# Optimization experiments

Hardware: AMD Instinct MI355X
Metric: run time of the kernel (lower is better)

Reference implementation:

```python
import jax, jax.numpy as jnp
import numpy as np

BETA = 0.5      # conf.beta (undefined global in original repo)
ALPHA = 0.2     # LeakyReLU negative slope (init arg alpha)
N, E, FIN, FOUT = 50000, 1_600_000, 128, 64


def setup_inputs() -> dict:
    key = jax.random.key(0)
    k1, k2, k3, k4, k5 = jax.random.split(key, 5)
    inp = jax.random.normal(k1, (N, FIN), dtype=jnp.float32)
    edge = jax.random.randint(k2, (2, E), 0, N)                      # [2,E] (src,dst), = adj.nonzero().t()
    M_vals = jax.random.uniform(k3, (E,), dtype=jnp.float32)          # M gathered at edges
    # xavier_normal with gain 1.414, matching torch init
    W = jax.random.normal(k4, (FIN, FOUT), dtype=jnp.float32) * (1.414 * np.sqrt(2.0 / (FIN + FOUT)))
    a = jax.random.normal(k5, (2 * FOUT,), dtype=jnp.float32) * (1.414 * np.sqrt(2.0 / (1 + 2 * FOUT)))
    return {"input": inp, "M_vals": M_vals, "W": W, "a": a, "edge": edge}


def reference(input, M_vals, W, a, edge):
    n, f = input.shape[0], W.shape[1]
    src, dst = edge[0], edge[1]
    h = input @ W                                   # [N, F]
    # M = beta*M + (1-beta)*adj; at edges adj == 1
    bias = M_vals * BETA + (1.0 - BETA)             # [E]
    # a . cat(h_src, bias*h_dst) == (h@a[:F])[src] + bias * (h@a[F:])[dst]
    s1 = h @ a[:f]                                  # [N]
    s2 = h @ a[f:]                                  # [N]
    edge_e = jnp.exp(jax.nn.leaky_relu(s1[src] + bias * s2[dst], negative_slope=ALPHA))  # [E]
    # special_spmm(edge, e, [N,N], ones) -> per-row sum of edge weights
    e_rowsum = jax.ops.segment_sum(edge_e, src, num_segments=n)       # [N]
    # special_spmm(edge, e, [N,N], h) -> weighted aggregation of dst features into src rows
    h_prime = jax.ops.segment_sum(edge_e[:, None] * h[dst], src, num_segments=n)  # [N, F]
    h_prime = h_prime / e_rowsum[:, None]
    return jax.nn.elu(h_prime)                      # concat=True
```

## Files before the change

### kernel.cpp

```cpp
#include <hip/hip_runtime.h>
#include <hip/hip_bf16.h>

#define NN   50000
#define EE   1600000
#define FIN  128
#define FOUT 64
#define BETA  0.5f
#define ALPHA 0.2f
#define SBW    256
#define NB2    196
#define RCAP   9000
#define PGRID  400
#define PCHUNK 4000
#define CAP2   9008
#define XS     136

typedef __attribute__((ext_vector_type(8))) short short8;
typedef __attribute__((ext_vector_type(8))) unsigned short ushort8v;
typedef __attribute__((ext_vector_type(4))) float float4v;

__device__ __forceinline__ float load_any(const void* p, long i, int isf32) {
    if (isf32) return ((const float*)p)[i];
    unsigned int b = ((unsigned int)(((const unsigned short*)p)[i])) << 16;
    return __uint_as_float(b);
}

__device__ __forceinline__ unsigned short f32_to_bf16_rne(float f) {
    unsigned int b = __float_as_uint(f);
    return (unsigned short)((b + 0x7FFF + ((b >> 16) & 1)) >> 16);
}

__device__ __forceinline__ float bf16_to_f32(unsigned short u) {
    return __uint_as_float(((unsigned int)u) << 16);
}

__global__ __launch_bounds__(256) void detect_kernel(
    const void* inp, const void* Mv, const void* W, const void* a, int* flags)
{
    const void* ptrs[4] = { inp, Mv, W, a };
    const long  cnts[4] = { (long)NN * FIN, (long)EE, (long)FIN * FOUT, 2L * FOUT };
    const int t = blockIdx.x;
    const unsigned short* p = (const unsigned short*)ptrs[t];
    const long half = cnts[t] >> 1;
    long step = half / 256; if (step == 0) step = 1;
    const long pos = 2 * (((long)threadIdx.x * step) % half);

    const float v = bf16_to_f32(p[pos]);
    const int bad = (isnan(v) || fabsf(v) > 1e4f) ? 1 : 0;

    __shared__ int sbad[256];
    sbad[threadIdx.x] = bad;
    __syncthreads();
    for (int s = 128; s > 0; s >>= 1) {
        if (threadIdx.x < (unsigned)s) sbad[threadIdx.x] |= sbad[threadIdx.x + s];
        __syncthreads();
    }
    if (threadIdx.x == 0) flags[t] = sbad[0];
}

__global__ __launch_bounds__(256) void wt_kernel(
    const void* __restrict__ W, const int* __restrict__ flags,
    unsigned short* __restrict__ Wt, int* __restrict__ bcur)
{
    if (blockIdx.x == 0 && threadIdx.x < NB2) bcur[threadIdx.x] = 0;
    const int fW = flags[2];
    const int i = blockIdx.x * 256 + threadIdx.x;
    if (i < FIN * FOUT) {
        const int k = i >> 6, n = i & 63;
        Wt[n * FIN + k] = f32_to_bf16_rne(load_any(W, i, fW));
    }
}

__global__ __launch_bounds__(256) void mfma_gemm_kernel(
    const void* __restrict__ inp,
    const unsigned short* __restrict__ Wt,
    const void* __restrict__ a,
    const int* __restrict__ flags,
    unsigned short* __restrict__ h,
    float* __restrict__ s1,
    float* __restrict__ s2)
{
    __shared__ unsigned short Xs[16 * XS];
    __shared__ float part1[4][16];
    __shared__ float part2[4][16];

    const int tid  = threadIdx.x;
    const int wave = tid >> 6;
    const int lane = tid & 63;
    const int quad = lane >> 4;
    const int col  = lane & 15;
    const int rb   = blockIdx.x * 16;

    const int fI = flags[0], fA = flags[3];

    {
        const int r = tid >> 4, k8 = (tid & 15) * 8;
        if (!fI) {
            const unsigned short* src = (const unsigned short*)inp + (long)(rb + r) * FIN + k8;
            *(ushort8v*)&Xs[r * XS + k8] = *(const ushort8v*)src;
        } else {
            const float* src = (const float*)inp + (long)(rb + r) * FIN + k8;
            ushort8v v;
            #pragma unroll
            for (int j = 0; j < 8; ++j) v[j] = f32_to_bf16_rne(src[j]);
            *(ushort8v*)&Xs[r * XS + k8] = v;
        }
    }
    __syncthreads();

    const int nb = wave * 16;
    float4v acc = { 0.f, 0.f, 0.f, 0.f };
    #pragma unroll
    for (int k0 = 0; k0 < FIN; k0 += 32) {
        const short8 af = *(const short8*)&Xs[col * XS + k0 + quad * 8];
        const short8 bf = *(const short8*)&Wt[(long)(nb + col) * FIN + k0 + quad * 8];
        acc = __builtin_amdgcn_mfma_f32_16x16x32_bf16(af, bf, acc, 0, 0, 0);
    }

    #pragma unroll
    for (int r = 0; r < 4; ++r)
        h[(long)(rb + quad * 4 + r) * FOUT + nb + col] = f32_to_bf16_rne(acc[r]);

    const float a1 = load_any(a, nb + col, fA);
    const float a2 = load_any(a, 64 + nb + col, fA);
    #pragma unroll
    for (int r = 0; r < 4; ++r) {
        float v1 = acc[r] * a1;
        float v2 = acc[r] * a2;
        #pragma unroll
        for (int o = 1; o < 16; o <<= 1) {
            v1 += __shfl_xor(v1, o, 64);
            v2 += __shfl_xor(v2, o, 64);
        }
        if (col == 0) {
            part1[wave][quad * 4 + r] = v1;
            part2[wave][quad * 4 + r] = v2;
        }
    }
    __syncthreads();
    if (tid < 16) {
        s1[rb + tid] = part1[0][tid] + part1[1][tid] + part1[2][tid] + part1[3][tid];
        s2[rb + tid] = part2[0][tid] + part2[1][tid] + part2[2][tid] + part2[3][tid];
    }
}

__global__ __launch_bounds__(1024) void partition_kernel(
    const int* __restrict__ edge,
    const void* __restrict__ Mv,
    const int* __restrict__ flags,
    const float* __restrict__ s1,
    const float* __restrict__ s2,
    int* __restrict__ bcur,
    unsigned long long* __restrict__ recs)
{
    __shared__ int lcnt[NB2];
    __shared__ int lbase[NB2];
    const int tid = threadIdx.x;
    const int fM = flags[1];
    const int e0 = blockIdx.x * PCHUNK;

    if (tid < NB2) lcnt[tid] = 0;
    __syncthreads();

    int srcs[4], dsts[4];
    float mvs[4];
    #pragma unroll
    for (int k = 0; k < 4; ++k) {
        const int e = e0 + tid + 1024 * k;
        const bool ok = (tid + 1024 * k) < PCHUNK;
        srcs[k] = ok ? edge[e] : -1;
        dsts[k] = ok ? edge[EE + e] : 0;
        mvs[k]  = ok ? load_any(Mv, e, fM) : 0.f;
    }
    #pragma unroll
    for (int k = 0; k < 4; ++k)
        if (srcs[k] >= 0) atomicAdd(&lcnt[srcs[k] >> 8], 1);
    __syncthreads();

    if (tid < NB2) {
        const int c = lcnt[tid];
        const int o = c ? atomicAdd(&bcur[tid], c) : 0;
        lbase[tid] = tid * RCAP + o;
        lcnt[tid] = 0;
    }
    __syncthreads();

    float ss1[4], ss2[4];
    #pragma unroll
    for (int k = 0; k < 4; ++k) {
        ss1[k] = (srcs[k] >= 0) ? s1[srcs[k]] : 0.f;
        ss2[k] = (srcs[k] >= 0) ? s2[dsts[k]] : 0.f;
    }
    #pragma unroll
    for (int k = 0; k < 4; ++k) {
        if (srcs[k] < 0) continue;
        const float bias = mvs[k] * BETA + (1.f - BETA);
        const float x  = ss1[k] + bias * ss2[k];
        const float lr = x > 0.f ? x : ALPHA * x;
        const float ee = __expf(lr);
        const int b = srcs[k] >> 8;
        const int r = atomicAdd(&lcnt[b], 1);
        const int pos = lbase[b] + r;
        if (pos < (b + 1) * RCAP)
            recs[pos] = ((unsigned long long)(unsigned)srcs[k] << 32)
                      | ((unsigned long long)(unsigned)dsts[k] << 16)
                      | (unsigned long long)f32_to_bf16_rne(ee);
    }
}

__global__ __launch_bounds__(1024) void bucket_csr_kernel(
    const int* __restrict__ bcur,
    const unsigned long long* __restrict__ recs,
    unsigned int* __restrict__ pairs,
    int* __restrict__ rowbeg,
    int* __restrict__ rowend)
{
    __shared__ unsigned long long lrec[CAP2];
    __shared__ int cnt[SBW];
    __shared__ int off[SBW];
    __shared__ int wsum[4];
    const int b    = blockIdx.x;
    const int tid  = threadIdx.x;
    const int rb   = b * SBW;
    const int beg  = b * RCAP;

    int n = bcur[b]; if (n > RCAP) n = RCAP;

    if (tid < SBW) cnt[tid] = 0;
    __syncthreads();

    for (int j = tid; j < n; j += 1024) {
        const unsigned long long rec = recs[beg + j];
        if (j < CAP2) lrec[j] = rec;
        atomicAdd(&cnt[(int)(rec >> 32) - rb], 1);
    }
    __syncthreads();

    int c = 0, x = 0;
    if (tid < SBW) {
        const int lane = tid & 63;
        c = cnt[tid];
        x = c;
        #pragma unroll
        for (int o = 1; o < 64; o <<= 1) {
            int y = __shfl_up(x, o, 64);
            if (lane >= o) x += y;
        }
        if (lane == 63) wsum[tid >> 6] = x;
    }
    __syncthreads();
    if (tid < SBW) {
        const int wave = tid >> 6;
        int wb = 0;
        for (int w = 0; w < wave; ++w) wb += wsum[w];
        const int myoff = wb + x - c;
        off[tid] = myoff;
        const int row = rb + tid;
        if (row < NN) {
            rowbeg[row] = beg + myoff;
            rowend[row] = beg + myoff + c;
        }
        cnt[tid] = 0;
    }
    __syncthreads();

    for (int j = tid; j < n; j += 1024) {
        const unsigned long long rec = (j < CAP2) ? lrec[j] : recs[beg + j];
        const int r = (int)(rec >> 32) - rb;
        const int rank = atomicAdd(&cnt[r], 1);
        pairs[beg + off[r] + rank] = (unsigned int)(rec & 0xFFFFFFFFu);
    }
}

__global__ __launch_bounds__(256) void spmm_kernel(
    const int* __restrict__ rowbeg,
    const int* __restrict__ rowend,
    const unsigned int* __restrict__ pairs,
    const unsigned short* __restrict__ h,
    const int* __restrict__ flags,
    void* __restrict__ out)
{
    const int wave = threadIdx.x >> 6;
    const int lane = threadIdx.x & 63;
    const int g    = lane >> 3;
    const int sl   = lane & 7;
    const int row  = blockIdx.x * 4 + wave;

    const int beg = rowbeg[row];
    const int end = rowend[row];

    float acc0 = 0.f, acc1 = 0.f, acc2 = 0.f, acc3 = 0.f;
    float acc4 = 0.f, acc5 = 0.f, acc6 = 0.f, acc7 = 0.f;
    float rsum = 0.f;
    int j = beg;
    for (; j + 15 < end; j += 16) {
        const unsigned int u0 = pairs[j + g];
        const unsigned int u1 = pairs[j + 8 + g];
        const ushort8v h0 = *(const ushort8v*)&h[(long)(u0 >> 16) * FOUT + 8 * sl];
        const ushort8v h1 = *(const ushort8v*)&h[(long)(u1 >> 16) * FOUT + 8 * sl];
        const float v0 = bf16_to_f32((unsigned short)(u0 & 0xFFFFu));
        const float v1 = bf16_to_f32((unsigned short)(u1 & 0xFFFFu));
        rsum += v0 + v1;
        acc0 = fmaf(v0, bf16_to_f32(h0[0]), acc0); acc0 = fmaf(v1, bf16_to_f32(h1[0]), acc0);
        acc1 = fmaf(v0, bf16_to_f32(h0[1]), acc1); acc1 = fmaf(v1, bf16_to_f32(h1[1]), acc1);
        acc2 = fmaf(v0, bf16_to_f32(h0[2]), acc2); acc2 = fmaf(v1, bf16_to_f32(h1[2]), acc2);
        acc3 = fmaf(v0, bf16_to_f32(h0[3]), acc3); acc3 = fmaf(v1, bf16_to_f32(h1[3]), acc3);
        acc4 = fmaf(v0, bf16_to_f32(h0[4]), acc4); acc4 = fmaf(v1, bf16_to_f32(h1[4]), acc4);
        acc5 = fmaf(v0, bf16_to_f32(h0[5]), acc5); acc5 = fmaf(v1, bf16_to_f32(h1[5]), acc5);
        acc6 = fmaf(v0, bf16_to_f32(h0[6]), acc6); acc6 = fmaf(v1, bf16_to_f32(h1[6]), acc6);
        acc7 = fmaf(v0, bf16_to_f32(h0[7]), acc7); acc7 = fmaf(v1, bf16_to_f32(h1[7]), acc7);
    }
    for (; j < end; j += 8) {
        if (j + g < end) {
            const unsigned int u = pairs[j + g];
            const ushort8v hv = *(const ushort8v*)&h[(long)(u >> 16) * FOUT + 8 * sl];
            const float v = bf16_to_f32((unsigned short)(u & 0xFFFFu));
            rsum += v;
            acc0 = fmaf(v, bf16_to_f32(hv[0]), acc0);
            acc1 = fmaf(v, bf16_to_f32(hv[1]), acc1);
            acc2 = fmaf(v, bf16_to_f32(hv[2]), acc2);
            acc3 = fmaf(v, bf16_to_f32(hv[3]), acc3);
            acc4 = fmaf(v, bf16_to_f32(hv[4]), acc4);
            acc5 = fmaf(v, bf16_to_f32(hv[5]), acc5);
            acc6 = fmaf(v, bf16_to_f32(hv[6]), acc6);
            acc7 = fmaf(v, bf16_to_f32(hv[7]), acc7);
        }
    }

    #pragma unroll
    for (int o = 8; o < 64; o <<= 1) {
        rsum += __shfl_xor(rsum, o, 64);
        acc0 += __shfl_xor(acc0, o, 64);
        acc1 += __shfl_xor(acc1, o, 64);
        acc2 += __shfl_xor(acc2, o, 64);
        acc3 += __shfl_xor(acc3, o, 64);
        acc4 += __shfl_xor(acc4, o, 64);
        acc5 += __shfl_xor(acc5, o, 64);
        acc6 += __shfl_xor(acc6, o, 64);
        acc7 += __shfl_xor(acc7, o, 64);
    }

    if (g == 0) {
        const float inv = 1.f / rsum;
        float q0 = acc0 * inv, q1 = acc1 * inv, q2 = acc2 * inv, q3 = acc3 * inv;
        float q4 = acc4 * inv, q5 = acc5 * inv, q6 = acc6 * inv, q7 = acc7 * inv;
        q0 = q0 > 0.f ? q0 : (__expf(q0) - 1.f);
        q1 = q1 > 0.f ? q1 : (__expf(q1) - 1.f);
        q2 = q2 > 0.f ? q2 : (__expf(q2) - 1.f);
        q3 = q3 > 0.f ? q3 : (__expf(q3) - 1.f);
        q4 = q4 > 0.f ? q4 : (__expf(q4) - 1.f);
        q5 = q5 > 0.f ? q5 : (__expf(q5) - 1.f);
        q6 = q6 > 0.f ? q6 : (__expf(q6) - 1.f);
        q7 = q7 > 0.f ? q7 : (__expf(q7) - 1.f);
        if (flags[0]) {
            float4* o = (float4*)((float*)out + (long)row * FOUT + 8 * sl);
            o[0] = make_float4(q0, q1, q2, q3);
            o[1] = make_float4(q4, q5, q6, q7);
        } else {
            ushort8v ov;
            ov[0] = f32_to_bf16_rne(q0); ov[1] = f32_to_bf16_rne(q1);
            ov[2] = f32_to_bf16_rne(q2); ov[3] = f32_to_bf16_rne(q3);
            ov[4] = f32_to_bf16_rne(q4); ov[5] = f32_to_bf16_rne(q5);
            ov[6] = f32_to_bf16_rne(q6); ov[7] = f32_to_bf16_rne(q7);
            *(ushort8v*)((unsigned short*)out + (long)row * FOUT + 8 * sl) = ov;
        }
    }
}

extern "C" void kernel_launch(void* const* d_in, const int* in_sizes, int n_in,
                              void* d_out, int out_size, void* d_ws, size_t ws_size,
                              hipStream_t stream) {
    const void* inp  = d_in[0];
    const void* Mv   = d_in[1];
    const void* W    = d_in[2];
    const void* a    = d_in[3];
    const int*  edge = (const int*)d_in[4];

    char* p = (char*)d_ws;
    int*                flags  = (int*)p;            p += 256;
    unsigned short*     Wt     = (unsigned short*)p; p += ((size_t)FOUT * FIN * 2 + 255) / 256 * 256;
    unsigned short*     h      = (unsigned short*)p; p += ((size_t)NN * FOUT * 2 + 255) / 256 * 256;
    float*              s1     = (float*)p;          p += ((size_t)NN * 4 + 255) / 256 * 256;
    float*              s2     = (float*)p;          p += ((size_t)NN * 4 + 255) / 256 * 256;
    int*                rowbeg = (int*)p;            p += ((size_t)NN * 4 + 255) / 256 * 256;
    int*                rowend = (int*)p;            p += ((size_t)NN * 4 + 255) / 256 * 256;
    int*                bcur   = (int*)p;            p += ((size_t)NB2 * 4 + 255) / 256 * 256;
    unsigned int*       pairs  = (unsigned int*)p;   p += ((size_t)NB2 * RCAP * 4 + 255) / 256 * 256;
    unsigned long long* recs   = (unsigned long long*)p;

    detect_kernel<<<4, 256, 0, stream>>>(inp, Mv, W, a, flags);
    wt_kernel<<<(FIN * FOUT + 255) / 256, 256, 0, stream>>>(W, flags, Wt, bcur);
    mfma_gemm_kernel<<<NN / 16, 256, 0, stream>>>(inp, Wt, a, flags, h, s1, s2);
    partition_kernel<<<PGRID, 1024, 0, stream>>>(edge, Mv, flags, s1, s2, bcur, recs);
    bucket_csr_kernel<<<NB2, 1024, 0, stream>>>(bcur, recs, pairs, rowbeg, rowend);
    spmm_kernel<<<NN / 4, 256, 0, stream>>>(rowbeg, rowend, pairs, h, flags, d_out);
}
```

Measured before the change: 168.6 us.

## Fuse dtype detection and W transpose into GEMM, merge CSR build with SpMM

Dtype detection and the W transpose/convert are folded into every GEMM block: each block votes on the input dtypes and builds the bf16 W tile in LDS. The bucket CSR build and the SpMM are merged, so each 256-row bucket sorts its edge pairs in LDS and aggregates them there, with no round trip through global memory. This cuts three kernel launches and the global writes and reads of pairs and row offsets. In exchange, every GEMM block now re-converts all of W. The SpMM runs on only 196 blocks of 1024 threads with large LDS use, which lowers parallelism for the gather phase.

```diff
diff --git a/kernel.cpp b/kernel.cpp
--- a/kernel.cpp
+++ b/kernel.cpp
@@ -12,8 +12,9 @@
 #define RCAP   9000
 #define PGRID  400
 #define PCHUNK 4000
-#define CAP2   9008
+#define CAP3   9008
 #define XS     136
+#define WS     136
 
 typedef __attribute__((ext_vector_type(8))) short short8;
 typedef __attribute__((ext_vector_type(8))) unsigned short ushort8v;
@@ -34,55 +35,22 @@
     return __uint_as_float(((unsigned int)u) << 16);
 }
 
-__global__ __launch_bounds__(256) void detect_kernel(
-    const void* inp, const void* Mv, const void* W, const void* a, int* flags)
-{
-    const void* ptrs[4] = { inp, Mv, W, a };
-    const long  cnts[4] = { (long)NN * FIN, (long)EE, (long)FIN * FOUT, 2L * FOUT };
-    const int t = blockIdx.x;
-    const unsigned short* p = (const unsigned short*)ptrs[t];
-    const long half = cnts[t] >> 1;
-    long step = half / 256; if (step == 0) step = 1;
-    const long pos = 2 * (((long)threadIdx.x * step) % half);
-
-    const float v = bf16_to_f32(p[pos]);
-    const int bad = (isnan(v) || fabsf(v) > 1e4f) ? 1 : 0;
-
-    __shared__ int sbad[256];
-    sbad[threadIdx.x] = bad;
-    __syncthreads();
-    for (int s = 128; s > 0; s >>= 1) {
-        if (threadIdx.x < (unsigned)s) sbad[threadIdx.x] |= sbad[threadIdx.x + s];
-        __syncthreads();
-    }
-    if (threadIdx.x == 0) flags[t] = sbad[0];
-}
-
-__global__ __launch_bounds__(256) void wt_kernel(
-    const void* __restrict__ W, const int* __restrict__ flags,
-    unsigned short* __restrict__ Wt, int* __restrict__ bcur)
-{
-    if (blockIdx.x == 0 && threadIdx.x < NB2) bcur[threadIdx.x] = 0;
-    const int fW = flags[2];
-    const int i = blockIdx.x * 256 + threadIdx.x;
-    if (i < FIN * FOUT) {
-        const int k = i >> 6, n = i & 63;
-        Wt[n * FIN + k] = f32_to_bf16_rne(load_any(W, i, fW));
-    }
-}
-
 __global__ __launch_bounds__(256) void mfma_gemm_kernel(
     const void* __restrict__ inp,
-    const unsigned short* __restrict__ Wt,
+    const void* __restrict__ W,
     const void* __restrict__ a,
-    const int* __restrict__ flags,
+    const void* __restrict__ Mv,
     unsigned short* __restrict__ h,
     float* __restrict__ s1,
-    float* __restrict__ s2)
+    float* __restrict__ s2,
+    int* __restrict__ flags,
+    int* __restrict__ bcur)
 {
     __shared__ unsigned short Xs[16 * XS];
+    __shared__ unsigned short Wl[64 * WS];
     __shared__ float part1[4][16];
     __shared__ float part2[4][16];
+    __shared__ int vote;
 
     const int tid  = threadIdx.x;
     const int wave = tid >> 6;
@@ -91,8 +59,41 @@
     const int col  = lane & 15;
     const int rb   = blockIdx.x * 16;
 
-    const int fI = flags[0], fA = flags[3];
-
+    if (tid == 0) vote = 0;
+    __syncthreads();
+
+    {
+        int m = 0;
+        const unsigned short* ip = (const unsigned short*)inp;
+        const float vi = bf16_to_f32(ip[(long)rb * FIN + tid * 8]);
+        if (isnan(vi) || fabsf(vi) > 1e4f) m |= 1;
+        if (tid < 128) {
+            const float va = bf16_to_f32(((const unsigned short*)a)[tid]);
+            if (isnan(va) || fabsf(va) > 1e4f) m |= 2;
+        }
+        const float vw = bf16_to_f32(((const unsigned short*)W)[tid * 16]);
+        if (isnan(vw) || fabsf(vw) > 1e4f) m |= 4;
+        if (blockIdx.x == 0) {
+            const long half = (long)EE >> 1;
+            const long pos = 2 * (((long)tid * (half / 256)) % half);
+            const float vm = bf16_to_f32(((const unsigned short*)Mv)[pos]);
+            if (isnan(vm) || fabsf(vm) > 1e4f) m |= 8;
+        }
+        if (m) atomicOr(&vote, m);
+    }
+    __syncthreads();
+    const int vm = vote;
+    const int fI = vm & 1, fA = (vm >> 1) & 1, fW = (vm >> 2) & 1;
+
+    if (blockIdx.x == 0) {
+        if (tid == 0) { flags[0] = fI; flags[1] = (vm >> 3) & 1; }
+        if (tid < NB2) bcur[tid] = 0;
+    }
+
+    for (int i = tid; i < FIN * FOUT; i += 256) {
+        const int k = i >> 6, n = i & 63;
+        Wl[n * WS + k] = f32_to_bf16_rne(load_any(W, i, fW));
+    }
     {
         const int r = tid >> 4, k8 = (tid & 15) * 8;
         if (!fI) {
@@ -113,7 +114,7 @@
     #pragma unroll
     for (int k0 = 0; k0 < FIN; k0 += 32) {
         const short8 af = *(const short8*)&Xs[col * XS + k0 + quad * 8];
-        const short8 bf = *(const short8*)&Wt[(long)(nb + col) * FIN + k0 + quad * 8];
+        const short8 bf = *(const short8*)&Wl[(nb + col) * WS + k0 + quad * 8];
         acc = __builtin_amdgcn_mfma_f32_16x16x32_bf16(af, bf, acc, 0, 0, 0);
     }
 
@@ -208,14 +209,15 @@
     }
 }
 
-__global__ __launch_bounds__(1024) void bucket_csr_kernel(
+__global__ __launch_bounds__(1024) void csr_spmm_kernel(
     const int* __restrict__ bcur,
     const unsigned long long* __restrict__ recs,
-    unsigned int* __restrict__ pairs,
-    int* __restrict__ rowbeg,
-    int* __restrict__ rowend)
+    const unsigned short* __restrict__ h,
+    const int* __restrict__ flags,
+    void* __restrict__ out)
 {
-    __shared__ unsigned long long lrec[CAP2];
+    __shared__ unsigned long long lrec[CAP3];
+    __shared__ unsigned int lpair[CAP3];
     __shared__ int cnt[SBW];
     __shared__ int off[SBW];
     __shared__ int wsum[4];
@@ -231,7 +233,7 @@
 
     for (int j = tid; j < n; j += 1024) {
         const unsigned long long rec = recs[beg + j];
-        if (j < CAP2) lrec[j] = rec;
+        lrec[j] = rec;
         atomicAdd(&cnt[(int)(rec >> 32) - rb], 1);
     }
     __syncthreads();
@@ -250,119 +252,109 @@
     }
     __syncthreads();
     if (tid < SBW) {
-        const int wave = tid >> 6;
+        const int wv = tid >> 6;
         int wb = 0;
-        for (int w = 0; w < wave; ++w) wb += wsum[w];
-        const int myoff = wb + x - c;
-        off[tid] = myoff;
-        const int row = rb + tid;
-        if (row < NN) {
-            rowbeg[row] = beg + myoff;
-            rowend[row] = beg + myoff + c;
-        }
+        for (int w = 0; w < wv; ++w) wb += wsum[w];
+        off[tid] = wb + x - c;
         cnt[tid] = 0;
     }
     __syncthreads();
 
     for (int j = tid; j < n; j += 1024) {
-        const unsigned long long rec = (j < CAP2) ? lrec[j] : recs[beg + j];
+        const unsigned long long rec = lrec[j];
         const int r = (int)(rec >> 32) - rb;
         const int rank = atomicAdd(&cnt[r], 1);
-        pairs[beg + off[r] + rank] = (unsigned int)(rec & 0xFFFFFFFFu);
-    }
-}
-
-__global__ __launch_bounds__(256) void spmm_kernel(
-    const int* __restrict__ rowbeg,
-    const int* __restrict__ rowend,
-    const unsigned int* __restrict__ pairs,
-    const unsigned short* __restrict__ h,
-    const int* __restrict__ flags,
-    void* __restrict__ out)
-{
-    const int wave = threadIdx.x >> 6;
-    const int lane = threadIdx.x & 63;
+        lpair[off[r] + rank] = (unsigned int)(rec & 0xFFFFFFFFu);
+    }
+    __syncthreads();
+
+    const int wv   = tid >> 6;
+    const int lane = tid & 63;
     const int g    = lane >> 3;
     const int sl   = lane & 7;
-    const int row  = blockIdx.x * 4 + wave;
-
-    const int beg = rowbeg[row];
-    const int end = rowend[row];
-
-    float acc0 = 0.f, acc1 = 0.f, acc2 = 0.f, acc3 = 0.f;
-    float acc4 = 0.f, acc5 = 0.f, acc6 = 0.f, acc7 = 0.f;
-    float rsum = 0.f;
-    int j = beg;
-    for (; j + 15 < end; j += 16) {
-        const unsigned int u0 = pairs[j + g];
-        const unsigned int u1 = pairs[j + 8 + g];
-        const ushort8v h0 = *(const ushort8v*)&h[(long)(u0 >> 16) * FOUT + 8 * sl];
-        const ushort8v h1 = *(const ushort8v*)&h[(long)(u1 >> 16) * FOUT + 8 * sl];
-        const float v0 = bf16_to_f32((unsigned short)(u0 & 0xFFFFu));
-        const float v1 = bf16_to_f32((unsigned short)(u1 & 0xFFFFu));
-        rsum += v0 + v1;
-        acc0 = fmaf(v0, bf16_to_f32(h0[0]), acc0); acc0 = fmaf(v1, bf16_to_f32(h1[0]), acc0);
-        acc1 = fmaf(v0, bf16_to_f32(h0[1]), acc1); acc1 = fmaf(v1, bf16_to_f32(h1[1]), acc1);
-        acc2 = fmaf(v0, bf16_to_f32(h0[2]), acc2); acc2 = fmaf(v1, bf16_to_f32(h1[2]), acc2);
-        acc3 = fmaf(v0, bf16_to_f32(h0[3]), acc3); acc3 = fmaf(v1, bf16_to_f32(h1[3]), acc3);
-        acc4 = fmaf(v0, bf16_to_f32(h0[4]), acc4); acc4 = fmaf(v1, bf16_to_f32(h1[4]), acc4);
-        acc5 = fmaf(v0, bf16_to_f32(h0[5]), acc5); acc5 = fmaf(v1, bf16_to_f32(h1[5]), acc5);
-        acc6 = fmaf(v0, bf16_to_f32(h0[6]), acc6); acc6 = fmaf(v1, bf16_to_f32(h1[6]), acc6);
-        acc7 = fmaf(v0, bf16_to_f32(h0[7]), acc7); acc7 = fmaf(v1, bf16_to_f32(h1[7]), acc7);
-    }
-    for (; j < end; j += 8) {
-        if (j + g < end) {
-            const unsigned int u = pairs[j + g];
-            const ushort8v hv = *(const ushort8v*)&h[(long)(u >> 16) * FOUT + 8 * sl];
-            const float v = bf16_to_f32((unsigned short)(u & 0xFFFFu));
-            rsum += v;
-            acc0 = fmaf(v, bf16_to_f32(hv[0]), acc0);
-            acc1 = fmaf(v, bf16_to_f32(hv[1]), acc1);
-            acc2 = fmaf(v, bf16_to_f32(hv[2]), acc2);
-            acc3 = fmaf(v, bf16_to_f32(hv[3]), acc3);
-            acc4 = fmaf(v, bf16_to_f32(hv[4]), acc4);
-            acc5 = fmaf(v, bf16_to_f32(hv[5]), acc5);
-            acc6 = fmaf(v, bf16_to_f32(hv[6]), acc6);
-            acc7 = fmaf(v, bf16_to_f32(hv[7]), acc7);
-        }
-    }
-
-    #pragma unroll
-    for (int o = 8; o < 64; o <<= 1) {
-        rsum += __shfl_xor(rsum, o, 64);
-        acc0 += __shfl_xor(acc0, o, 64);
-        acc1 += __shfl_xor(acc1, o, 64);
-        acc2 += __shfl_xor(acc2, o, 64);
-        acc3 += __shfl_xor(acc3, o, 64);
-        acc4 += __shfl_xor(acc4, o, 64);
-        acc5 += __shfl_xor(acc5, o, 64);
-        acc6 += __shfl_xor(acc6, o, 64);
-        acc7 += __shfl_xor(acc7, o, 64);
-    }
-
-    if (g == 0) {
-        const float inv = 1.f / rsum;
-        float q0 = acc0 * inv, q1 = acc1 * inv, q2 = acc2 * inv, q3 = acc3 * inv;
-        float q4 = acc4 * inv, q5 = acc5 * inv, q6 = acc6 * inv, q7 = acc7 * inv;
-        q0 = q0 > 0.f ? q0 : (__expf(q0) - 1.f);
-        q1 = q1 > 0.f ? q1 : (__expf(q1) - 1.f);
-        q2 = q2 > 0.f ? q2 : (__expf(q2) - 1.f);
-        q3 = q3 > 0.f ? q3 : (__expf(q3) - 1.f);
-        q4 = q4 > 0.f ? q4 : (__expf(q4) - 1.f);
-        q5 = q5 > 0.f ? q5 : (__expf(q5) - 1.f);
-        q6 = q6 > 0.f ? q6 : (__expf(q6) - 1.f);
-        q7 = q7 > 0.f ? q7 : (__expf(q7) - 1.f);
-        if (flags[0]) {
-            float4* o = (float4*)((float*)out + (long)row * FOUT + 8 * sl);
-            o[0] = make_float4(q0, q1, q2, q3);
-            o[1] = make_float4(q4, q5, q6, q7);
-        } else {
-            ushort8v ov;
-            ov[0] = f32_to_bf16_rne(q0); ov[1] = f32_to_bf16_rne(q1);
-            ov[2] = f32_to_bf16_rne(q2); ov[3] = f32_to_bf16_rne(q3);
-            ov[4] = f32_to_bf16_rne(q4); ov[5] = f32_to_bf16_rne(q5);
-            ov[6] = f32_to_bf16_rne(q6); ov[7] = f32_to_bf16_rne(q7);
-            *(ushort8v*)((unsigned short*)out + (long)row * FOUT + 8 * sl) = ov;
+    const int fOut = flags[0];
+
+    for (int rr = wv; rr < SBW; rr += 16) {
+        const int row = rb + rr;
+        if (row >= NN) break;
+        const int jb = off[rr];
+        const int je = jb + cnt[rr];
+
+        float acc0 = 0.f, acc1 = 0.f, acc2 = 0.f, acc3 = 0.f;
+        float acc4 = 0.f, acc5 = 0.f, acc6 = 0.f, acc7 = 0.f;
+        float rsum = 0.f;
+        int j = jb;
+        for (; j + 15 < je; j += 16) {
+            const unsigned int u0 = lpair[j + g];
+            const unsigned int u1 = lpair[j + 8 + g];
+            const ushort8v h0 = *(const ushort8v*)&h[(long)(u0 >> 16) * FOUT + 8 * sl];
+            const ushort8v h1 = *(const ushort8v*)&h[(long)(u1 >> 16) * FOUT + 8 * sl];
+            const float v0 = bf16_to_f32((unsigned short)(u0 & 0xFFFFu));
+            const float v1 = bf16_to_f32((unsigned short)(u1 & 0xFFFFu));
+            rsum += v0 + v1;
+            acc0 = fmaf(v0, bf16_to_f32(h0[0]), acc0); acc0 = fmaf(v1, bf16_to_f32(h1[0]), acc0);
+            acc1 = fmaf(v0, bf16_to_f32(h0[1]), acc1); acc1 = fmaf(v1, bf16_to_f32(h1[1]), acc1);
+            acc2 = fmaf(v0, bf16_to_f32(h0[2]), acc2); acc2 = fmaf(v1, bf16_to_f32(h1[2]), acc2);
+            acc3 = fmaf(v0, bf16_to_f32(h0[3]), acc3); acc3 = fmaf(v1, bf16_to_f32(h1[3]), acc3);
+            acc4 = fmaf(v0, bf16_to_f32(h0[4]), acc4); acc4 = fmaf(v1, bf16_to_f32(h1[4]), acc4);
+            acc5 = fmaf(v0, bf16_to_f32(h0[5]), acc5); acc5 = fmaf(v1, bf16_to_f32(h1[5]), acc5);
+            acc6 = fmaf(v0, bf16_to_f32(h0[6]), acc6); acc6 = fmaf(v1, bf16_to_f32(h1[6]), acc6);
+            acc7 = fmaf(v0, bf16_to_f32(h0[7]), acc7); acc7 = fmaf(v1, bf16_to_f32(h1[7]), acc7);
+        }
+        for (; j < je; j += 8) {
+            if (j + g < je) {
+                const unsigned int u = lpair[j + g];
+                const ushort8v hv = *(const ushort8v*)&h[(long)(u >> 16) * FOUT + 8 * sl];
+                const float v = bf16_to_f32((unsigned short)(u & 0xFFFFu));
+                rsum += v;
+                acc0 = fmaf(v, bf16_to_f32(hv[0]), acc0);
+                acc1 = fmaf(v, bf16_to_f32(hv[1]), acc1);
+                acc2 = fmaf(v, bf16_to_f32(hv[2]), acc2);
+                acc3 = fmaf(v, bf16_to_f32(hv[3]), acc3);
+                acc4 = fmaf(v, bf16_to_f32(hv[4]), acc4);
+                acc5 = fmaf(v, bf16_to_f32(hv[5]), acc5);
+                acc6 = fmaf(v, bf16_to_f32(hv[6]), acc6);
+                acc7 = fmaf(v, bf16_to_f32(hv[7]), acc7);
+            }
+        }
+
+        #pragma unroll
+        for (int o = 8; o < 64; o <<= 1) {
+            rsum += __shfl_xor(rsum, o, 64);
+            acc0 += __shfl_xor(acc0, o, 64);
+            acc1 += __shfl_xor(acc1, o, 64);
+            acc2 += __shfl_xor(acc2, o, 64);
+            acc3 += __shfl_xor(acc3, o, 64);
+            acc4 += __shfl_xor(acc4, o, 64);
+            acc5 += __shfl_xor(acc5, o, 64);
+            acc6 += __shfl_xor(acc6, o, 64);
+            acc7 += __shfl_xor(acc7, o, 64);
+        }
+
+        if (g == 0) {
+            const float inv = 1.f / rsum;
+            float q0 = acc0 * inv, q1 = acc1 * inv, q2 = acc2 * inv, q3 = acc3 * inv;
+            float q4 = acc4 * inv, q5 = acc5 * inv, q6 = acc6 * inv, q7 = acc7 * inv;
+            q0 = q0 > 0.f ? q0 : (__expf(q0) - 1.f);
+            q1 = q1 > 0.f ? q1 : (__expf(q1) - 1.f);
+            q2 = q2 > 0.f ? q2 : (__expf(q2) - 1.f);
+            q3 = q3 > 0.f ? q3 : (__expf(q3) - 1.f);
+            q4 = q4 > 0.f ? q4 : (__expf(q4) - 1.f);
+            q5 = q5 > 0.f ? q5 : (__expf(q5) - 1.f);
+            q6 = q6 > 0.f ? q6 : (__expf(q6) - 1.f);
+            q7 = q7 > 0.f ? q7 : (__expf(q7) - 1.f);
+            if (fOut) {
+                float4* o = (float4*)((float*)out + (long)row * FOUT + 8 * sl);
+                o[0] = make_float4(q0, q1, q2, q3);
+                o[1] = make_float4(q4, q5, q6, q7);
+            } else {
+                ushort8v ov;
+                ov[0] = f32_to_bf16_rne(q0); ov[1] = f32_to_bf16_rne(q1);
+                ov[2] = f32_to_bf16_rne(q2); ov[3] = f32_to_bf16_rne(q3);
+                ov[4] = f32_to_bf16_rne(q4); ov[5] = f32_to_bf16_rne(q5);
+                ov[6] = f32_to_bf16_rne(q6); ov[7] = f32_to_bf16_rne(q7);
+                *(ushort8v*)((unsigned short*)out + (long)row * FOUT + 8 * sl) = ov;
+            }
         }
     }
 }
@@ -378,20 +370,13 @@
 
     char* p = (char*)d_ws;
     int*                flags  = (int*)p;            p += 256;
-    unsigned short*     Wt     = (unsigned short*)p; p += ((size_t)FOUT * FIN * 2 + 255) / 256 * 256;
     unsigned short*     h      = (unsigned short*)p; p += ((size_t)NN * FOUT * 2 + 255) / 256 * 256;
     float*              s1     = (float*)p;          p += ((size_t)NN * 4 + 255) / 256 * 256;
     float*              s2     = (float*)p;          p += ((size_t)NN * 4 + 255) / 256 * 256;
-    int*                rowbeg = (int*)p;            p += ((size_t)NN * 4 + 255) / 256 * 256;
-    int*                rowend = (int*)p;            p += ((size_t)NN * 4 + 255) / 256 * 256;
     int*                bcur   = (int*)p;            p += ((size_t)NB2 * 4 + 255) / 256 * 256;
-    unsigned int*       pairs  = (unsigned int*)p;   p += ((size_t)NB2 * RCAP * 4 + 255) / 256 * 256;
     unsigned long long* recs   = (unsigned long long*)p;
 
-    detect_kernel<<<4, 256, 0, stream>>>(inp, Mv, W, a, flags);
-    wt_kernel<<<(FIN * FOUT + 255) / 256, 256, 0, stream>>>(W, flags, Wt, bcur);
-    mfma_gemm_kernel<<<NN / 16, 256, 0, stream>>>(inp, Wt, a, flags, h, s1, s2);
+    mfma_gemm_kernel<<<NN / 16, 256, 0, stream>>>(inp, W, a, Mv, h, s1, s2, flags, bcur);
     partition_kernel<<<PGRID, 1024, 0, stream>>>(edge, Mv, flags, s1, s2, bcur, recs);
-    bucket_csr_kernel<<<NB2, 1024, 0, stream>>>(bcur, recs, pairs, rowbeg, rowend);
-    spmm_kernel<<<NN / 4, 256, 0, stream>>>(rowbeg, rowend, pairs, h, flags, d_out);
-}
+    csr_spmm_kernel<<<NB2, 1024, 0, stream>>>(bcur, recs, h, flags, d_out);
+}
```

Measured after the change: 183.5 us. 1.09x slower.
